# Kernel tuning notes

Hardware: AMD Instinct MI355X
Metric: run time of the kernel (lower is better)

Reference implementation:

```python
import jax, jax.numpy as jnp
import numpy as np

B, T, C = 4, 2048, 768
H = 12
D = C // H  # head dim 64

def setup_inputs() -> dict:
    key = jax.random.key(0)
    ks = jax.random.split(key, 6)
    scale = 1.0 / np.sqrt(C)
    x = jax.random.normal(ks[0], (B, T, C), dtype=jnp.float32)
    attention_mask = jax.random.randint(ks[1], (B, T), 0, 2, dtype=jnp.int64)
    Wqkv = jax.random.normal(ks[2], (C, 3 * C), dtype=jnp.float32) * scale
    bqkv = jax.random.normal(ks[3], (3 * C,), dtype=jnp.float32) * 0.02
    Wo = jax.random.normal(ks[4], (C, C), dtype=jnp.float32) * scale
    bo = jax.random.normal(ks[5], (C,), dtype=jnp.float32) * 0.02
    return {"x": x, "attention_mask": attention_mask, "Wqkv": Wqkv,
            "bqkv": bqkv, "Wo": Wo, "bo": bo}

def reference(x, attention_mask, Wqkv, bqkv, Wo, bo):
    # fused QKV projection: [B,T,3C]
    qkv = jnp.einsum('btc,cd->btd', x, Wqkv) + bqkv
    q, k, v = jnp.split(qkv, 3, axis=-1)
    # reshape to [B,H,T,D]
    q = q.reshape(B, T, H, D).transpose(0, 2, 1, 3)
    k = k.reshape(B, T, H, D).transpose(0, 2, 1, 3)
    v = v.reshape(B, T, H, D).transpose(0, 2, 1, 3)
    # module quirk: True (attended) where attention_mask == 0
    keep = (attention_mask == 0)[:, None, None, :]  # [B,1,1,T]
    scores = jnp.einsum('bhqd,bhkd->bhqk', q, k) / np.sqrt(D)
    scores = jnp.where(keep, scores, jnp.finfo(scores.dtype).min)
    probs = jax.nn.softmax(scores, axis=-1)
    context = jnp.einsum('bhqk,bhkd->bhqd', probs, v)
    context = context.transpose(0, 2, 1, 3).reshape(B, T, C)
    return jnp.einsum('btc,cd->btd', context, Wo) + bo
```

## Files before the change

### kernel.cpp

```cpp
#include <hip/hip_runtime.h>
#include <stdint.h>

#define AS1 __attribute__((address_space(1)))
#define AS3 __attribute__((address_space(3)))

typedef _Float16 f16;
typedef _Float16 f16x8 __attribute__((ext_vector_type(8)));
typedef _Float16 f16x4 __attribute__((ext_vector_type(4)));
typedef _Float16 f16x2 __attribute__((ext_vector_type(2)));
typedef float    f32x4  __attribute__((ext_vector_type(4)));
typedef float    f32x16 __attribute__((ext_vector_type(16)));

#define B_  4
#define T_  2048
#define C_  768
#define H_  12
#define D_  64
#define M_  (B_*T_)
#define N1_ (3*C_)

__device__ __forceinline__ void g2l16(const void* g, void* l) {
  __builtin_amdgcn_global_load_lds((const AS1 void*)g, (AS3 void*)l, 16, 0, 0);
}

__device__ __forceinline__ f32x4 fzero4() { f32x4 z = {0.f, 0.f, 0.f, 0.f}; return z; }

__device__ __forceinline__ f16x2 pk_f16(float a, float b) {
  auto t = __builtin_amdgcn_cvt_pkrtz(a, b);
  return *(f16x2*)&t;
}

__global__ __launch_bounds__(256)
void transpose_cvt_k(const float* __restrict__ in, f16* __restrict__ out, int R, int C) {
  __shared__ float tile[32][33];
  const int tx = threadIdx.x & 31, ty = threadIdx.x >> 5;
  const int c0 = blockIdx.x * 32, r0 = blockIdx.y * 32;
#pragma unroll
  for (int i = 0; i < 32; i += 8)
    tile[ty + i][tx] = in[(long)(r0 + ty + i) * C + c0 + tx];
  __syncthreads();
#pragma unroll
  for (int i = 0; i < 32; i += 8)
    out[(long)(c0 + ty + i) * R + r0 + tx] = (f16)tile[tx][ty + i];
}

__global__ __launch_bounds__(256)
void convert_f32_f16(const float* __restrict__ in, f16* __restrict__ out) {
  const int i = (blockIdx.x * 256 + threadIdx.x) * 4;
  const float4 v = *(const float4*)(in + i);
  f16x4 o = {(f16)v.x, (f16)v.y, (f16)v.z, (f16)v.w};
  *(f16x4*)(out + i) = o;
}

__global__ __launch_bounds__(256)
void init_idx_kernel(int* __restrict__ idx, int* __restrict__ cnt) {
  const int g = blockIdx.x * 256 + threadIdx.x;
  idx[g] = 0;
  if (g < B_) cnt[g] = 0;
}

__global__ __launch_bounds__(256)
void compact_kernel(const int* __restrict__ mask, int* __restrict__ idx,
                    int* __restrict__ cnt) {
  const int b = blockIdx.y;
  const int t = blockIdx.x * 256 + threadIdx.x;
  if (mask[b * T_ + t] == 0) {
    const int s = atomicAdd(&cnt[b], 1);
    idx[b * T_ + s] = t;
  }
}

__global__ __launch_bounds__(256)
void build_vt(const f16* __restrict__ Vc, const int* __restrict__ cnt,
              f16* __restrict__ vt) {
  __shared__ f16 tile[32][33];
  const int z = blockIdx.z, b = z / H_, h = z % H_;
  const int s0 = blockIdx.x * 32, d0 = blockIdx.y * 32;
  if (s0 >= ((cnt[b] + 63) & ~63)) return;
  const int tx = threadIdx.x & 31, ty = threadIdx.x >> 5;
  f16* dst = vt + (long)z * D_ * T_;
#pragma unroll
  for (int i = 0; i < 32; i += 8)
    tile[ty + i][tx] = Vc[(long)(b * T_ + s0 + ty + i) * C_ + h * D_ + d0 + tx];
  __syncthreads();
#pragma unroll
  for (int i = 0; i < 32; i += 8)
    dst[(long)(d0 + ty + i) * T_ + s0 + tx] = tile[tx][ty + i];
}

template <typename OutT>
__global__ __launch_bounds__(256)
void gemm_bias_kernel(const f16* __restrict__ A, const f16* __restrict__ Bt,
                      const float* __restrict__ bias, OutT* __restrict__ Cc,
                      int K, int ldc) {
  __shared__ f16 lA[128 * 32];
  __shared__ f16 lB[128 * 32];
  const int tid = threadIdx.x;
  const int n0 = blockIdx.x * 128, m0 = blockIdx.y * 128;
  const int lane = tid & 63, w = tid >> 6;
  const int wm = (w & 1) * 64, wn = (w >> 1) * 64;
  const int r15 = lane & 15, q4 = lane >> 4;

  const int c0 = tid, c1 = 256 + tid;
  const int ar0 = c0 >> 2, ak0 = (c0 & 3) * 8;
  const int ar1 = c1 >> 2, ak1 = (c1 & 3) * 8;
  const f16* Ab = A + (long)m0 * K;
  const f16* Bb = Bt + (long)n0 * K;

  f32x4 acc[4][4];
#pragma unroll
  for (int i = 0; i < 4; i++)
#pragma unroll
    for (int j = 0; j < 4; j++) acc[i][j] = fzero4();

  for (int kb = 0; kb < K; kb += 32) {
    g2l16(Ab + (long)ar0 * K + kb + ak0, &lA[c0 * 8]);
    g2l16(Ab + (long)ar1 * K + kb + ak1, &lA[c1 * 8]);
    g2l16(Bb + (long)ar0 * K + kb + ak0, &lB[c0 * 8]);
    g2l16(Bb + (long)ar1 * K + kb + ak1, &lB[c1 * 8]);
    __syncthreads();
    f16x8 af[4], bfv[4];
#pragma unroll
    for (int mi = 0; mi < 4; mi++)
      af[mi] = *(const f16x8*)&lA[(wm + mi * 16 + r15) * 32 + q4 * 8];
#pragma unroll
    for (int ni = 0; ni < 4; ni++)
      bfv[ni] = *(const f16x8*)&lB[(wn + ni * 16 + r15) * 32 + q4 * 8];
#pragma unroll
    for (int mi = 0; mi < 4; mi++)
#pragma unroll
      for (int ni = 0; ni < 4; ni++)
        acc[mi][ni] = __builtin_amdgcn_mfma_f32_16x16x32_f16(af[mi], bfv[ni], acc[mi][ni], 0, 0, 0);
    __syncthreads();
  }

#pragma unroll
  for (int ni = 0; ni < 4; ni++) {
    const int col = n0 + wn + ni * 16 + r15;
    const float bs = bias[col];
#pragma unroll
    for (int mi = 0; mi < 4; mi++) {
#pragma unroll
      for (int r = 0; r < 4; r++) {
        const int row = m0 + wm + mi * 16 + q4 * 4 + r;
        Cc[(long)row * ldc + col] = (OutT)(acc[mi][ni][r] + bs);
      }
    }
  }
}

__global__ __launch_bounds__(512, 2)
void gemm_qkv256(const f16* __restrict__ A, const f16* __restrict__ Bt,
                 const float* __restrict__ bias, f16* __restrict__ Qb,
                 f16* __restrict__ Kc, f16* __restrict__ Vc,
                 const int* __restrict__ idx, const int* __restrict__ cnt) {
  const int K = C_;
  __shared__ f16 lA[2 * 256 * 64];
  __shared__ f16 lB[2 * 256 * 64];
  const int tid = threadIdx.x;
  const int nb = blockIdx.x;
  const int mb = blockIdx.y;
  const bool isQ = nb < 3;

  int b = 0, s0 = 0;
  if (!isQ) {
    b = mb >> 3;
    s0 = (mb & 7) * 256;
    if (s0 >= cnt[b]) return;
  }

  const int lane = tid & 63, w = tid >> 6;
  const int wmi = w >> 2, wni = w & 3;
  const int r15 = lane & 15, q4 = lane >> 4;
  const int rx = (r15 & 7) * 8;

  const int trow = tid >> 3;
  const int koffsw = (((tid & 7) ^ (trow & 7)) * 8);
  const f16* pA[4];
  const f16* pB[4];
#pragma unroll
  for (int i = 0; i < 4; i++) {
    const int ri = i * 64 + trow;
    long grow;
    if (isQ) grow = (long)mb * 256 + ri;
    else     grow = (long)b * T_ + idx[b * T_ + s0 + ri];
    pA[i] = A + grow * K + koffsw;
    pB[i] = Bt + (long)(nb * 256 + ri) * K + koffsw;
  }
  const int lofs = tid * 8;

  f32x4 acc[8][4];
#pragma unroll
  for (int i = 0; i < 8; i++)
#pragma unroll
    for (int j = 0; j < 4; j++) acc[i][j] = fzero4();

#define STAGE_QKV(bufsel, kb) do {                                        \
  const int lb = (bufsel) * 16384;                                        \
  _Pragma("unroll")                                                       \
  for (int i = 0; i < 4; i++) {                                           \
    g2l16(pA[i] + (kb), &lA[lb + i * 4096 + lofs]);                       \
    g2l16(pB[i] + (kb), &lB[lb + i * 4096 + lofs]);                       \
  }                                                                       \
} while (0)

#define COMPUTE_QKV(bufsel) do {                                          \
  const int lb = (bufsel) * 16384;                                        \
  _Pragma("unroll")                                                       \
  for (int kh = 0; kh < 2; kh++) {                                        \
    const int cofs = (kh * 32 + q4 * 8) ^ rx;                             \
    f16x8 af[8], bf[4];                                                   \
    _Pragma("unroll")                                                     \
    for (int mi = 0; mi < 8; mi++)                                        \
      af[mi] = *(const f16x8*)&lA[lb + (wmi * 128 + mi * 16 + r15) * 64 + cofs]; \
    _Pragma("unroll")                                                     \
    for (int ni = 0; ni < 4; ni++)                                        \
      bf[ni] = *(const f16x8*)&lB[lb + (wni * 64 + ni * 16 + r15) * 64 + cofs];  \
    _Pragma("unroll")                                                     \
    for (int mi = 0; mi < 8; mi++)                                        \
      _Pragma("unroll")                                                   \
      for (int ni = 0; ni < 4; ni++)                                      \
        acc[mi][ni] = __builtin_amdgcn_mfma_f32_16x16x32_f16(af[mi], bf[ni], acc[mi][ni], 0, 0, 0); \
  }                                                                       \
} while (0)

  STAGE_QKV(0, 0);
  __syncthreads();

  int cur = 0;
  const int NT = K / 64;
  for (int t = 0; t < NT - 1; t++) {
    STAGE_QKV(cur ^ 1, (t + 1) * 64);
    COMPUTE_QKV(cur);
    __syncthreads();
    cur ^= 1;
  }
  COMPUTE_QKV(cur);

#undef STAGE_QKV
#undef COMPUTE_QKV

#pragma unroll
  for (int ni = 0; ni < 4; ni++) {
    const int cN = nb * 256 + wni * 64 + ni * 16 + r15;
    const float bs = bias[cN];
    f16* outp;
    int ocol;
    long rowbase;
    if (isQ)               { outp = Qb; ocol = cN;        rowbase = (long)mb * 256; }
    else if (cN < 2 * C_)  { outp = Kc; ocol = cN - C_;   rowbase = (long)b * T_ + s0; }
    else                   { outp = Vc; ocol = cN - 2*C_; rowbase = (long)b * T_ + s0; }
#pragma unroll
    for (int mi = 0; mi < 8; mi++) {
#pragma unroll
      for (int r = 0; r < 4; r++) {
        const long row = rowbase + wmi * 128 + mi * 16 + q4 * 4 + r;
        outp[row * C_ + ocol] = (f16)(acc[mi][ni][r] + bs);
      }
    }
  }
}

__global__ __launch_bounds__(256, 4)
void attn_kernel(const f16* __restrict__ Qb, const f16* __restrict__ Kc,
                 const f16* __restrict__ vtc, const int* __restrict__ cnt,
                 f16* __restrict__ ctx) {
  const int LDS_ = 72;
  __shared__ f16 QPs[128 * 72];
  __shared__ f16 Ks[64 * 72], Vs[64 * 72];
  const int tid = threadIdx.x, lane = tid & 63, w = tid >> 6;
  const int l31 = lane & 31, hh = lane >> 5;
  const int bh = blockIdx.y, b = bh / H_, h = bh % H_;
  const int q0 = blockIdx.x * 128;
  const f16* Qg = Qb + (long)(b * T_ + q0) * C_ + h * D_;
  const f16* Kbase = Kc + (long)b * T_ * C_ + h * D_;
  const f16* Vg = vtc + (long)bh * D_ * T_;
  const int nk = cnt[b];
  const int nkt = (nk + 63) >> 6;

  const f16 qsc = (f16)0.18033688f;
#pragma unroll
  for (int i = 0; i < 4; i++) {
    int c = i * 256 + tid, r = c >> 3, dcq = (c & 7) * 8;
    f16x8 v = *(const f16x8*)(Qg + (long)r * C_ + dcq);
#pragma unroll
    for (int j = 0; j < 8; j++) v[j] = v[j] * qsc;
    *(f16x8*)&QPs[r * LDS_ + dcq] = v;
  }
  __syncthreads();
  f16x8 bq[4];
#pragma unroll
  for (int j = 0; j < 4; j++)
    bq[j] = *(const f16x8*)&QPs[(w * 32 + l31) * LDS_ + j * 16 + hh * 8];

  const int r0 = tid >> 3, r1 = 32 + (tid >> 3), dc = (tid & 7) * 8;

  float l_acc = 0.f;
  f32x16 O[2];
#pragma unroll
  for (int dt = 0; dt < 2; dt++)
#pragma unroll
    for (int r = 0; r < 16; r++) O[dt][r] = 0.f;

  for (int kt = 0; kt < (nkt << 6); kt += 64) {
    __syncthreads();
    {
      f16x8 kv0 = *(const f16x8*)(Kbase + (long)(kt + r0) * C_ + dc);
      f16x8 kv1 = *(const f16x8*)(Kbase + (long)(kt + r1) * C_ + dc);
      f16x8 vv0 = *(const f16x8*)(Vg + (long)r0 * T_ + kt + dc);
      f16x8 vv1 = *(const f16x8*)(Vg + (long)r1 * T_ + kt + dc);
      *(f16x8*)&Ks[r0 * LDS_ + dc] = kv0;
      *(f16x8*)&Ks[r1 * LDS_ + dc] = kv1;
      *(f16x8*)&Vs[r0 * LDS_ + dc] = vv0;
      *(f16x8*)&Vs[r1 * LDS_ + dc] = vv1;
    }
    __syncthreads();

    const bool full = (kt + 64 <= nk);
#pragma unroll
    for (int ktile = 0; ktile < 2; ktile++) {
      f32x16 acc;
      if (full) {
#pragma unroll
        for (int r = 0; r < 16; r++) acc[r] = 0.f;
      } else {
        const int kbase = kt + ktile * 32 + hh * 4;
#pragma unroll
        for (int g = 0; g < 4; g++)
#pragma unroll
          for (int i = 0; i < 4; i++)
            acc[4 * g + i] = (kbase + 8 * g + i < nk) ? 0.f : -1e30f;
      }
#pragma unroll
      for (int j = 0; j < 4; j++) {
        f16x8 ak = *(const f16x8*)&Ks[(ktile * 32 + l31) * LDS_ + j * 16 + hh * 8];
        acc = __builtin_amdgcn_mfma_f32_32x32x16_f16(ak, bq[j], acc, 0, 0, 0);
      }
#pragma unroll
      for (int g = 0; g < 4; g++) {
        const float p0 = __builtin_amdgcn_exp2f(acc[4 * g + 0]);
        const float p1 = __builtin_amdgcn_exp2f(acc[4 * g + 1]);
        const float p2 = __builtin_amdgcn_exp2f(acc[4 * g + 2]);
        const float p3 = __builtin_amdgcn_exp2f(acc[4 * g + 3]);
        l_acc += (p0 + p1) + (p2 + p3);
        const f16x2 lo = pk_f16(p0, p1), hi = pk_f16(p2, p3);
        f16x4 pv; pv[0] = lo[0]; pv[1] = lo[1]; pv[2] = hi[0]; pv[3] = hi[1];
        *(f16x4*)&QPs[(w * 32 + l31) * LDS_ + ktile * 32 + g * 8 + hh * 4] = pv;
      }
    }
    asm volatile("s_waitcnt lgkmcnt(0)" ::: "memory");

#pragma unroll
    for (int j = 0; j < 4; j++) {
      f16x8 pa = *(const f16x8*)&QPs[(w * 32 + l31) * LDS_ + j * 16 + hh * 8];
#pragma unroll
      for (int dt = 0; dt < 2; dt++) {
        f16x8 vb = *(const f16x8*)&Vs[(dt * 32 + l31) * LDS_ + j * 16 + hh * 8];
        O[dt] = __builtin_amdgcn_mfma_f32_32x32x16_f16(pa, vb, O[dt], 0, 0, 0);
      }
    }
  }

  l_acc += __shfl_xor(l_acc, 32);
  float* Lw = (float*)&QPs[(w * 32) * LDS_];
  asm volatile("s_waitcnt lgkmcnt(0)" ::: "memory");
  if (hh == 0) Lw[l31] = l_acc;
  asm volatile("s_waitcnt lgkmcnt(0)" ::: "memory");
#pragma unroll
  for (int g = 0; g < 4; g++) {
    const f32x4 lv = *(const f32x4*)&Lw[g * 8 + hh * 4];
#pragma unroll
    for (int i = 0; i < 4; i++) {
      const float inv = 1.f / lv[i];
      const int row = b * T_ + q0 + w * 32 + g * 8 + hh * 4 + i;
#pragma unroll
      for (int dt = 0; dt < 2; dt++)
        ctx[(long)row * C_ + h * D_ + dt * 32 + l31] = (f16)(O[dt][4 * g + i] * inv);
    }
  }
}

extern "C" void kernel_launch(void* const* d_in, const int* in_sizes, int n_in,
                              void* d_out, int out_size, void* d_ws, size_t ws_size,
                              hipStream_t stream) {
  (void)in_sizes; (void)n_in; (void)out_size; (void)ws_size;
  const float* x    = (const float*)d_in[0];
  const int*   mask = (const int*)  d_in[1];
  const float* Wqkv = (const float*)d_in[2];
  const float* bqkv = (const float*)d_in[3];
  const float* Wo   = (const float*)d_in[4];
  const float* bo   = (const float*)d_in[5];
  float* out = (float*)d_out;

  char* ws = (char*)d_ws;
  const size_t OFF_WQKVT = 0;
  const size_t OFF_WOT   = OFF_WQKVT + 3538944;
  const size_t OFF_Q     = OFF_WOT + 1179648;
  const size_t OFF_KC    = OFF_Q + 12582912;
  const size_t OFF_VC    = OFF_KC + 12582912;
  const size_t OFF_VT    = OFF_VC + 12582912;
  const size_t OFF_XH    = OFF_VT + 12582912;
  const size_t OFF_IDX   = OFF_XH + 12582912;
  const size_t OFF_CNT   = OFF_IDX + 32768;
  f16* WqkvT = (f16*)(ws + OFF_WQKVT);
  f16* WoT   = (f16*)(ws + OFF_WOT);
  f16* Qb    = (f16*)(ws + OFF_Q);
  f16* Kc    = (f16*)(ws + OFF_KC);
  f16* Vc    = (f16*)(ws + OFF_VC);
  f16* Vtc   = (f16*)(ws + OFF_VT);
  f16* xh    = (f16*)(ws + OFF_XH);
  f16* ctx   = (f16*)(ws + OFF_XH);
  int* idx   = (int*)(ws + OFF_IDX);
  int* cnt   = (int*)(ws + OFF_CNT);

  transpose_cvt_k<<<dim3(72, 24), 256, 0, stream>>>(Wqkv, WqkvT, 768, 2304);
  transpose_cvt_k<<<dim3(24, 24), 256, 0, stream>>>(Wo, WoT, 768, 768);
  convert_f32_f16<<<dim3(M_ * C_ / 1024), 256, 0, stream>>>(x, xh);
  init_idx_kernel<<<dim3(B_ * T_ / 256), 256, 0, stream>>>(idx, cnt);
  compact_kernel<<<dim3(T_ / 256, B_), 256, 0, stream>>>(mask, idx, cnt);
  gemm_qkv256<<<dim3(9, 32), 512, 0, stream>>>(xh, WqkvT, bqkv, Qb, Kc, Vc, idx, cnt);
  build_vt<<<dim3(64, 2, 48), 256, 0, stream>>>(Vc, cnt, Vtc);
  attn_kernel<<<dim3(16, 48), 256, 0, stream>>>(Qb, Kc, Vtc, cnt, ctx);
  gemm_bias_kernel<float><<<dim3(6, 64), 256, 0, stream>>>(ctx, WoT, bo, out, 768, 768);
}
```

Measured before the change: 201.1 us.

## Double-buffer K/V via async LDS loads, keep P in registers with permlane swap

The attention kernel now streams K and V tiles into double-buffered, XOR-swizzled LDS using global_load_lds, so the next tile's load overlaps compute on the current one. The softmax probabilities are moved into MFMA A-operand layout with permlane32_swap instead of a round trip through LDS. Q is loaded straight into registers, and blocks are remapped so each XCD handles a contiguous set of heads to improve L2 locality. LDS use and register pressure change, and the swizzle and permlane layout must match the MFMA fragment layout exactly.

```diff
diff --git a/kernel.cpp b/kernel.cpp
--- a/kernel.cpp
+++ b/kernel.cpp
@@ -10,6 +10,8 @@
 typedef _Float16 f16x2 __attribute__((ext_vector_type(2)));
 typedef float    f32x4  __attribute__((ext_vector_type(4)));
 typedef float    f32x16 __attribute__((ext_vector_type(16)));
+typedef uint32_t u32x4  __attribute__((ext_vector_type(4)));
+typedef uint32_t u32x2  __attribute__((ext_vector_type(2)));
 
 #define B_  4
 #define T_  2048
@@ -25,9 +27,14 @@
 
 __device__ __forceinline__ f32x4 fzero4() { f32x4 z = {0.f, 0.f, 0.f, 0.f}; return z; }
 
-__device__ __forceinline__ f16x2 pk_f16(float a, float b) {
+__device__ __forceinline__ uint32_t pk_u32(float a, float b) {
   auto t = __builtin_amdgcn_cvt_pkrtz(a, b);
-  return *(f16x2*)&t;
+  return *(uint32_t*)&t;
+}
+
+__device__ __forceinline__ void pl32swap(uint32_t& d, uint32_t& s) {
+  u32x2 r = __builtin_amdgcn_permlane32_swap(d, s, false, false);
+  d = r[0]; s = r[1];
 }
 
 __global__ __launch_bounds__(256)
@@ -265,13 +272,18 @@
 void attn_kernel(const f16* __restrict__ Qb, const f16* __restrict__ Kc,
                  const f16* __restrict__ vtc, const int* __restrict__ cnt,
                  f16* __restrict__ ctx) {
-  const int LDS_ = 72;
-  __shared__ f16 QPs[128 * 72];
-  __shared__ f16 Ks[64 * 72], Vs[64 * 72];
+  __shared__ f16 Ks[2][64 * 64];
+  __shared__ f16 Vs[2][64 * 64];
+  __shared__ float Ls[4][32];
   const int tid = threadIdx.x, lane = tid & 63, w = tid >> 6;
   const int l31 = lane & 31, hh = lane >> 5;
-  const int bh = blockIdx.y, b = bh / H_, h = bh % H_;
-  const int q0 = blockIdx.x * 128;
+
+  const int g = blockIdx.y * 16 + blockIdx.x;
+  const int xcd = g & 7, local = g >> 3;
+  const int bh = xcd * 6 + (local >> 4);
+  const int q0 = (local & 15) * 128;
+  const int b = bh / H_, h = bh % H_;
+
   const f16* Qg = Qb + (long)(b * T_ + q0) * C_ + h * D_;
   const f16* Kbase = Kc + (long)b * T_ * C_ + h * D_;
   const f16* Vg = vtc + (long)bh * D_ * T_;
@@ -279,21 +291,30 @@
   const int nkt = (nk + 63) >> 6;
 
   const f16 qsc = (f16)0.18033688f;
-#pragma unroll
-  for (int i = 0; i < 4; i++) {
-    int c = i * 256 + tid, r = c >> 3, dcq = (c & 7) * 8;
-    f16x8 v = *(const f16x8*)(Qg + (long)r * C_ + dcq);
-#pragma unroll
-    for (int j = 0; j < 8; j++) v[j] = v[j] * qsc;
-    *(f16x8*)&QPs[r * LDS_ + dcq] = v;
-  }
-  __syncthreads();
   f16x8 bq[4];
 #pragma unroll
-  for (int j = 0; j < 4; j++)
-    bq[j] = *(const f16x8*)&QPs[(w * 32 + l31) * LDS_ + j * 16 + hh * 8];
-
-  const int r0 = tid >> 3, r1 = 32 + (tid >> 3), dc = (tid & 7) * 8;
+  for (int j = 0; j < 4; j++) {
+    f16x8 v = *(const f16x8*)(Qg + (long)(w * 32 + l31) * C_ + j * 16 + hh * 8);
+#pragma unroll
+    for (int e = 0; e < 8; e++) v[e] = v[e] * qsc;
+    bq[j] = v;
+  }
+
+  const int r_0 = w * 16 + (lane >> 3);
+  const int sc = ((lane & 7) ^ (r_0 & 7)) * 8;
+  const f16* Ksrc0 = Kbase + (long)r_0 * C_ + sc;
+  const f16* Ksrc1 = Kbase + (long)(r_0 + 8) * C_ + sc;
+  const f16* Vsrc0 = Vg + (long)r_0 * T_ + sc;
+  const f16* Vsrc1 = Vg + (long)(r_0 + 8) * T_ + sc;
+  const int ld0 = w * 1024 + lane * 8;
+  const int ld1 = ld0 + 512;
+
+#define ATTN_STAGE(bs, kt) do {                                  \
+    g2l16(Ksrc0 + (long)(kt) * C_, &Ks[bs][ld0]);                \
+    g2l16(Ksrc1 + (long)(kt) * C_, &Ks[bs][ld1]);                \
+    g2l16(Vsrc0 + (kt), &Vs[bs][ld0]);                           \
+    g2l16(Vsrc1 + (kt), &Vs[bs][ld1]);                           \
+  } while (0)
 
   float l_acc = 0.f;
   f32x16 O[2];
@@ -302,80 +323,89 @@
 #pragma unroll
     for (int r = 0; r < 16; r++) O[dt][r] = 0.f;
 
-  for (int kt = 0; kt < (nkt << 6); kt += 64) {
-    __syncthreads();
-    {
-      f16x8 kv0 = *(const f16x8*)(Kbase + (long)(kt + r0) * C_ + dc);
-      f16x8 kv1 = *(const f16x8*)(Kbase + (long)(kt + r1) * C_ + dc);
-      f16x8 vv0 = *(const f16x8*)(Vg + (long)r0 * T_ + kt + dc);
-      f16x8 vv1 = *(const f16x8*)(Vg + (long)r1 * T_ + kt + dc);
-      *(f16x8*)&Ks[r0 * LDS_ + dc] = kv0;
-      *(f16x8*)&Ks[r1 * LDS_ + dc] = kv1;
-      *(f16x8*)&Vs[r0 * LDS_ + dc] = vv0;
-      *(f16x8*)&Vs[r1 * LDS_ + dc] = vv1;
-    }
-    __syncthreads();
-
+  const int swz = l31 & 7;
+
+  ATTN_STAGE(0, 0);
+  __syncthreads();
+
+  int cur = 0;
+  for (int t = 0; t < nkt; t++) {
+    const int kt = t * 64;
+    if (t + 1 < nkt) ATTN_STAGE(cur ^ 1, kt + 64);
+
+    u32x4 paw[4];
     const bool full = (kt + 64 <= nk);
 #pragma unroll
-    for (int ktile = 0; ktile < 2; ktile++) {
+    for (int t2 = 0; t2 < 2; t2++) {
       f32x16 acc;
       if (full) {
 #pragma unroll
         for (int r = 0; r < 16; r++) acc[r] = 0.f;
       } else {
-        const int kbase = kt + ktile * 32 + hh * 4;
-#pragma unroll
-        for (int g = 0; g < 4; g++)
+        const int kbase = kt + t2 * 32 + hh * 4;
+#pragma unroll
+        for (int g4 = 0; g4 < 4; g4++)
 #pragma unroll
           for (int i = 0; i < 4; i++)
-            acc[4 * g + i] = (kbase + 8 * g + i < nk) ? 0.f : -1e30f;
+            acc[4 * g4 + i] = (kbase + 8 * g4 + i < nk) ? 0.f : -1e30f;
       }
 #pragma unroll
       for (int j = 0; j < 4; j++) {
-        f16x8 ak = *(const f16x8*)&Ks[(ktile * 32 + l31) * LDS_ + j * 16 + hh * 8];
+        f16x8 ak = *(const f16x8*)&Ks[cur][(t2 * 32 + l31) * 64 + (((j * 2 + hh) ^ swz) << 3)];
         acc = __builtin_amdgcn_mfma_f32_32x32x16_f16(ak, bq[j], acc, 0, 0, 0);
       }
-#pragma unroll
-      for (int g = 0; g < 4; g++) {
-        const float p0 = __builtin_amdgcn_exp2f(acc[4 * g + 0]);
-        const float p1 = __builtin_amdgcn_exp2f(acc[4 * g + 1]);
-        const float p2 = __builtin_amdgcn_exp2f(acc[4 * g + 2]);
-        const float p3 = __builtin_amdgcn_exp2f(acc[4 * g + 3]);
+      uint32_t wg[4], xg[4];
+#pragma unroll
+      for (int g4 = 0; g4 < 4; g4++) {
+        const float p0 = __builtin_amdgcn_exp2f(acc[4 * g4 + 0]);
+        const float p1 = __builtin_amdgcn_exp2f(acc[4 * g4 + 1]);
+        const float p2 = __builtin_amdgcn_exp2f(acc[4 * g4 + 2]);
+        const float p3 = __builtin_amdgcn_exp2f(acc[4 * g4 + 3]);
         l_acc += (p0 + p1) + (p2 + p3);
-        const f16x2 lo = pk_f16(p0, p1), hi = pk_f16(p2, p3);
-        f16x4 pv; pv[0] = lo[0]; pv[1] = lo[1]; pv[2] = hi[0]; pv[3] = hi[1];
-        *(f16x4*)&QPs[(w * 32 + l31) * LDS_ + ktile * 32 + g * 8 + hh * 4] = pv;
+        wg[g4] = pk_u32(p0, p1);
+        xg[g4] = pk_u32(p2, p3);
+      }
+#pragma unroll
+      for (int jl = 0; jl < 2; jl++) {
+        uint32_t w0 = wg[2 * jl], w2v = wg[2 * jl + 1];
+        uint32_t w1 = xg[2 * jl], w3v = xg[2 * jl + 1];
+        pl32swap(w0, w2v);
+        pl32swap(w1, w3v);
+        paw[2 * t2 + jl][0] = w0;  paw[2 * t2 + jl][1] = w1;
+        paw[2 * t2 + jl][2] = w2v; paw[2 * t2 + jl][3] = w3v;
       }
     }
-    asm volatile("s_waitcnt lgkmcnt(0)" ::: "memory");
 
 #pragma unroll
     for (int j = 0; j < 4; j++) {
-      f16x8 pa = *(const f16x8*)&QPs[(w * 32 + l31) * LDS_ + j * 16 + hh * 8];
+      const f16x8 pa = *(const f16x8*)&paw[j];
 #pragma unroll
       for (int dt = 0; dt < 2; dt++) {
-        f16x8 vb = *(const f16x8*)&Vs[(dt * 32 + l31) * LDS_ + j * 16 + hh * 8];
+        const int vrow = dt * 32 + l31;
+        f16x8 vb = *(const f16x8*)&Vs[cur][vrow * 64 + (((j * 2 + hh) ^ swz) << 3)];
         O[dt] = __builtin_amdgcn_mfma_f32_32x32x16_f16(pa, vb, O[dt], 0, 0, 0);
       }
     }
-  }
+
+    __syncthreads();
+    cur ^= 1;
+  }
+#undef ATTN_STAGE
 
   l_acc += __shfl_xor(l_acc, 32);
-  float* Lw = (float*)&QPs[(w * 32) * LDS_];
   asm volatile("s_waitcnt lgkmcnt(0)" ::: "memory");
-  if (hh == 0) Lw[l31] = l_acc;
+  if (hh == 0) Ls[w][l31] = l_acc;
   asm volatile("s_waitcnt lgkmcnt(0)" ::: "memory");
 #pragma unroll
-  for (int g = 0; g < 4; g++) {
-    const f32x4 lv = *(const f32x4*)&Lw[g * 8 + hh * 4];
+  for (int g4 = 0; g4 < 4; g4++) {
+    const f32x4 lv = *(const f32x4*)&Ls[w][g4 * 8 + hh * 4];
 #pragma unroll
     for (int i = 0; i < 4; i++) {
       const float inv = 1.f / lv[i];
-      const int row = b * T_ + q0 + w * 32 + g * 8 + hh * 4 + i;
+      const int row = b * T_ + q0 + w * 32 + g4 * 8 + hh * 4 + i;
 #pragma unroll
       for (int dt = 0; dt < 2; dt++)
-        ctx[(long)row * C_ + h * D_ + dt * 32 + l31] = (f16)(O[dt][4 * g + i] * inv);
+        ctx[(long)row * C_ + h * D_ + dt * 32 + l31] = (f16)(O[dt][4 * g4 + i] * inv);
     }
   }
 }
```

New measurement: 195.3 us. 2.9% less time.
